# Kernel optimization log

Hardware: AMD Instinct MI355X
Metric: run time of the kernel (lower is better)

Reference implementation:

```python
import jax, jax.numpy as jnp
import numpy as np

N_NODES = 10000
N_EDGES = 160000
HIDDEN = 128
NGAUSS = 100
NF = 64
N_CONV = 2


def setup_inputs() -> dict:
    key = jax.random.key(0)
    ks = jax.random.split(key, 10)
    h = jax.random.normal(ks[0], (N_NODES, HIDDEN), dtype=jnp.float32)
    edge_index = jax.random.randint(ks[1], (2, N_EDGES), 0, N_NODES, dtype=jnp.int64)
    edge_weight = jax.random.uniform(ks[2], (N_EDGES,), dtype=jnp.float32)
    edge_attr = jax.random.normal(ks[3], (N_EDGES, NGAUSS), dtype=jnp.float32)
    data = jnp.zeros((1,), dtype=jnp.float32)
    s = 0.05
    lin0_w = jax.random.normal(ks[4], (HIDDEN, NF), dtype=jnp.float32) * s
    lin0_b = jnp.zeros((NF,), dtype=jnp.float32)
    nn_w1 = jax.random.normal(ks[5], (NGAUSS, HIDDEN), dtype=jnp.float32) * s
    nn_b1 = jnp.zeros((HIDDEN,), dtype=jnp.float32)
    nn_w2 = jax.random.normal(ks[6], (HIDDEN, NF * NF), dtype=jnp.float32) * s
    nn_b2 = jnp.zeros((NF * NF,), dtype=jnp.float32)
    root_w = jax.random.normal(ks[7], (NF, NF), dtype=jnp.float32) * s
    conv_b = jnp.zeros((NF,), dtype=jnp.float32)
    return {"h": h, "edge_index": edge_index, "edge_weight": edge_weight,
            "edge_attr": edge_attr, "data": data,
            "lin0_w": lin0_w, "lin0_b": lin0_b,
            "nn_w1": nn_w1, "nn_b1": nn_b1, "nn_w2": nn_w2, "nn_b2": nn_b2,
            "root_w": root_w, "conv_b": conv_b}


def reference(h, edge_index, edge_weight, edge_attr, data,
              lin0_w, lin0_b, nn_w1, nn_b1, nn_w2, nn_b2, root_w, conv_b):
    # lin0 + relu -> node features x: [N, nf]
    x = jax.nn.relu(h @ lin0_w + lin0_b)

    # edge network: per-edge weight matrix W_e: [E, nf, nf]
    hidden = jax.nn.relu(edge_attr @ nn_w1 + nn_b1)
    W_e = (hidden @ nn_w2 + nn_b2).reshape(N_EDGES, NF, NF)

    src = edge_index[0]  # message source (x_j)
    dst = edge_index[1]  # aggregation target (i)

    # in-degree for mean aggregation (0-degree nodes -> 0 output)
    deg = jax.ops.segment_sum(jnp.ones((N_EDGES,), x.dtype), dst, num_segments=N_NODES)
    inv_deg = (1.0 / jnp.maximum(deg, 1.0))[:, None]  # [N, 1]

    # n_conv applications of the SAME NNConv (shared weights)
    for _ in range(N_CONV):
        msg = jnp.einsum('ei,eio->eo', x[src], W_e)  # gather + per-edge matvec
        agg = jax.ops.segment_sum(msg, dst, num_segments=N_NODES) * inv_deg
        x = agg + x @ root_w + conv_b
    return x
```

## Files before the change

### kernel.cpp

```cpp
#include <hip/hip_runtime.h>

#define N_NODES 10000
#define N_EDGES 160000
#define HID 128
#define NG 100
#define NF 64
#define NIO 4096
#define NJ 8192
#define M_PAD 10240

#define PREP_EA 10000
#define PREP_LIN0 (PREP_EA + 2500)
#define PREP_WPT (PREP_LIN0 + 2112)

typedef short bf16x8 __attribute__((ext_vector_type(8)));
typedef float f32x4 __attribute__((ext_vector_type(4)));

__device__ __forceinline__ unsigned short f2b(float f) {
    unsigned int u = __float_as_uint(f);
    u += 0x7fffu + ((u >> 16) & 1u);
    return (unsigned short)(u >> 16);
}
__device__ __forceinline__ float b2f(unsigned short s) { return __uint_as_float((unsigned int)s << 16); }

__device__ __forceinline__ long fidx64(int row, int k) {
    return (long)(row >> 4) * 1024 + (k >> 5) * 512 + ((((k >> 3) & 3) * 16 + (row & 15))) * 8 + (k & 7);
}
__device__ __forceinline__ long fidx128(int row, int k) {
    return (long)(row >> 4) * 2048 + (k >> 5) * 512 + ((((k >> 3) & 3) * 16 + (row & 15))) * 8 + (k & 7);
}

__global__ void hist_kernel(const int* __restrict__ src, const int* __restrict__ dst,
                            float* __restrict__ deg, int* __restrict__ cnt) {
    int e = blockIdx.x * 256 + threadIdx.x;
    if (e < N_EDGES) {
        atomicAdd(&deg[dst[e]], 1.0f);
        atomicAdd(&cnt[src[e]], 1);
    }
}

#define SCAN_C 40
__global__ void scan_kernel(const int* __restrict__ cnt, const float* __restrict__ deg,
                            int* __restrict__ rowptr, float* __restrict__ invd) {
    __shared__ int wsum[4];
    int t = threadIdx.x, wv = t >> 6, l = t & 63;
    int base_i = t * SCAN_C;
    int loc[SCAN_C];
    int sum = 0;
#pragma unroll
    for (int j = 0; j < SCAN_C; ++j) {
        int g = base_i + j;
        int v = (g < N_NODES) ? cnt[g] : 0;
        loc[j] = sum;
        sum += v;
    }
    int incl = sum;
    for (int off = 1; off < 64; off <<= 1) {
        int v = __shfl_up(incl, off);
        if (l >= off) incl += v;
    }
    if (l == 63) wsum[wv] = incl;
    __syncthreads();
    int wbase = 0;
#pragma unroll
    for (int w = 0; w < 4; ++w) wbase += (w < wv) ? wsum[w] : 0;
    int tbase = wbase + incl - sum;
#pragma unroll
    for (int j = 0; j < SCAN_C; ++j) {
        int g = base_i + j;
        if (g <= N_NODES) rowptr[g] = tbase + loc[j];
        if (g < N_NODES) invd[g] = 1.0f / fmaxf(deg[g], 1.0f);
    }
}

__global__ void scatter_kernel(const int* __restrict__ src, const int* __restrict__ dst,
                               const int* __restrict__ rowptr, int* __restrict__ fill,
                               int* __restrict__ edgeOf, int* __restrict__ dstp) {
    int e = blockIdx.x * 256 + threadIdx.x;
    if (e < N_EDGES) {
        int s = src[e];
        int r = rowptr[s] + atomicAdd(&fill[s], 1);
        edgeOf[r] = e;
        dstp[r] = dst[e];
    }
}

__global__ void prep_kernel(const float* __restrict__ ea, const int* __restrict__ edgeOf,
                            unsigned short* __restrict__ eah,
                            const float* __restrict__ h, const float* __restrict__ lw,
                            const float* __restrict__ lb, const float* __restrict__ b2,
                            float* __restrict__ x, unsigned short* __restrict__ xh,
                            float* __restrict__ xb2,
                            const float* __restrict__ w1, const float* __restrict__ w2,
                            unsigned short* __restrict__ w1h, unsigned short* __restrict__ w2h) {
    int bid = blockIdx.x;
    if (bid < PREP_EA) {
        int t = threadIdx.x;
        int r15 = t & 15, ksl = t >> 4;
        int ks = ksl >> 2, lk = ksl & 3;
        long rank = (long)bid * 16 + r15;
        long e = edgeOf[rank];
        int c0 = ks * 32 + lk * 8;
        unsigned int uh[4];
#pragma unroll
        for (int p = 0; p < 4; ++p) {
            float v0 = (c0 + 2 * p < NG) ? ea[e * NG + c0 + 2 * p] : 0.0f;
            float v1 = (c0 + 2 * p + 1 < NG) ? ea[e * NG + c0 + 2 * p + 1] : 0.0f;
            uh[p] = ((unsigned int)f2b(v1) << 16) | f2b(v0);
        }
        long idx = (long)bid * 2048 + ks * 512 + (lk * 16 + r15) * 8;
        *(uint4*)(eah + idx) = make_uint4(uh[0], uh[1], uh[2], uh[3]);
    } else if (bid < PREP_LIN0) {
        int wv = threadIdx.x >> 6, l = threadIdx.x & 63;
        int n = (bid - PREP_EA) * 4 + wv;
        float h0 = h[n * HID + l];
        float h1 = h[n * HID + 64 + l];
        float acc = lb[l];
#pragma unroll
        for (int i = 0; i < 64; ++i) {
            acc += __shfl(h0, i) * lw[i * NF + l];
            acc += __shfl(h1, i) * lw[(64 + i) * NF + l];
        }
        float v = fmaxf(acc, 0.0f);
        x[n * NF + l] = v;
        xh[fidx64(n, l)] = f2b(v);
        float xb = 0.0f;
#pragma unroll
        for (int i = 0; i < 64; ++i) xb += __shfl(v, i) * b2[i * 64 + l];
        xb2[n * NF + l] = xb;
    } else {
        int id = (bid - PREP_LIN0) * 256 + threadIdx.x;
        if (id < HID * HID) {
            int k = id & 127, c = id >> 7;
            float v = (k < NG) ? w1[k * HID + c] : 0.0f;
            w1h[fidx128(c, k)] = f2b(v);
        } else {
            int id2 = id - HID * HID;
            int i = id2 & 63, j = id2 >> 6;
            int o = j >> 7, k = j & 127;
            w2h[fidx64(j, i)] = f2b(w2[k * NIO + i * 64 + o]);
        }
    }
}

__launch_bounds__(256)
__global__ void hgemm_kernel(const unsigned short* __restrict__ eah,
                             const unsigned short* __restrict__ w1h,
                             const float* __restrict__ b1, unsigned short* __restrict__ hidp) {
    __shared__ float stg[4][1056];
    const int tid = threadIdx.x, wv = tid >> 6, l = tid & 63;
    const long grow = (long)blockIdx.x * 128;
    const int wr = (wv >> 1) * 64, wc = (wv & 1) * 64;
    const long apan0 = (grow >> 4) + (wr >> 4);
    const long bpan0 = (wc >> 4);

    f32x4 acc[4][4] = {};
#pragma unroll
    for (int ks = 0; ks < 4; ++ks) {
        bf16x8 a[4], b[4];
#pragma unroll
        for (int m = 0; m < 4; ++m)
            a[m] = *(const bf16x8*)(eah + (apan0 + m) * 2048 + ks * 512 + (long)l * 8);
#pragma unroll
        for (int n = 0; n < 4; ++n)
            b[n] = *(const bf16x8*)(w1h + (bpan0 + n) * 2048 + ks * 512 + (long)l * 8);
#pragma unroll
        for (int m = 0; m < 4; ++m)
#pragma unroll
            for (int n = 0; n < 4; ++n)
                acc[m][n] = __builtin_amdgcn_mfma_f32_16x16x32_bf16(a[m], b[n], acc[m][n], 0, 0, 0);
    }

    float* s = stg[wv];
    int r8 = l >> 3, cg = l & 7;
#pragma unroll
    for (int m = 0; m < 4; ++m) {
#pragma unroll
        for (int n = 0; n < 4; ++n)
#pragma unroll
            for (int q = 0; q < 4; ++q)
                s[((l >> 4) * 4 + q) * 66 + n * 16 + (l & 15)] = acc[m][n][q];
#pragma unroll
        for (int it = 0; it < 2; ++it) {
            int row = it * 8 + r8;
            const float* sr = s + row * 66 + cg * 8;
            int colbase = wc + cg * 8;
            unsigned int u[4];
#pragma unroll
            for (int p = 0; p < 4; ++p) {
                float f0 = fmaxf(sr[2 * p] + b1[colbase + 2 * p], 0.0f);
                float f1 = fmaxf(sr[2 * p + 1] + b1[colbase + 2 * p + 1], 0.0f);
                u[p] = ((unsigned int)f2b(f1) << 16) | f2b(f0);
            }
            long R = grow + wr + m * 16 + row;
            *(uint4*)(hidp + R * HID + colbase) = make_uint4(u[0], u[1], u[2], u[3]);
        }
    }
}

__launch_bounds__(256)
__global__ void ygemm_kernel(const unsigned short* __restrict__ xh,
                             const unsigned short* __restrict__ wh,
                             unsigned short* __restrict__ y, int n0) {
    __shared__ float stg[4][1056];
    const int tid = threadIdx.x, wv = tid >> 6, l = tid & 63;
    const int grow = blockIdx.x * 128;
    const int col0base = blockIdx.y * 256;
    const int wr = (wv >> 1) * 64, wc = (wv & 1) * 64;
    const long apan0 = ((n0 + grow + wr) >> 4);
    const int r8 = l >> 3, cg = l & 7;

    bf16x8 a[2][4];
#pragma unroll
    for (int ks = 0; ks < 2; ++ks)
#pragma unroll
        for (int m = 0; m < 4; ++m)
            a[ks][m] = *(const bf16x8*)(xh + (apan0 + m) * 1024 + ks * 512 + (long)l * 8);

    for (int ct = 0; ct < 2; ++ct) {
        const int col0 = col0base + ct * 128;
        const long bpan0 = ((col0 + wc) >> 4);
        f32x4 acc[4][4] = {};
#pragma unroll
        for (int ks = 0; ks < 2; ++ks) {
            bf16x8 b[4];
#pragma unroll
            for (int n = 0; n < 4; ++n)
                b[n] = *(const bf16x8*)(wh + (bpan0 + n) * 1024 + ks * 512 + (long)l * 8);
#pragma unroll
            for (int m = 0; m < 4; ++m)
#pragma unroll
                for (int n = 0; n < 4; ++n)
                    acc[m][n] = __builtin_amdgcn_mfma_f32_16x16x32_bf16(a[ks][m], b[n], acc[m][n], 0, 0, 0);
        }

        float* s = stg[wv];
#pragma unroll
        for (int m = 0; m < 4; ++m) {
#pragma unroll
            for (int n = 0; n < 4; ++n)
#pragma unroll
                for (int q = 0; q < 4; ++q)
                    s[((l >> 4) * 4 + q) * 66 + n * 16 + (l & 15)] = acc[m][n][q];
#pragma unroll
            for (int it = 0; it < 2; ++it) {
                int row = it * 8 + r8;
                const float* sr = s + row * 66 + cg * 8;
                unsigned int u[4];
#pragma unroll
                for (int p = 0; p < 4; ++p)
                    u[p] = ((unsigned int)f2b(sr[2 * p + 1]) << 16) | f2b(sr[2 * p]);
                long R = grow + wr + m * 16 + row;
                *(uint4*)(y + R * NJ + col0 + wc + cg * 8) = make_uint4(u[0], u[1], u[2], u[3]);
            }
        }
    }
}

__global__ void matvec_mfma_kernel(const unsigned short* __restrict__ y,
                                   const unsigned short* __restrict__ hidp,
                                   const int* __restrict__ rowptr, const int* __restrict__ dstp,
                                   const float* __restrict__ xb2, float* __restrict__ agg,
                                   int n0, int n1) {
    int wv = threadIdx.x >> 6, l = threadIdx.x & 63;
    int s = n0 + blockIdx.x * 4 + wv;
    if (s >= n1) return;
    int r0 = rowptr[s], r1 = rowptr[s + 1];
    if (r0 == r1) return;
    int lc = l & 15, lk = l >> 4;

    const unsigned short* Ys = y + (long)(s - n0) * NJ;
    bf16x8 b[4][4];
    float xb2v[4];
#pragma unroll
    for (int og = 0; og < 4; ++og) {
        const unsigned short* Yo = Ys + (og * 16 + lc) * HID + lk * 8;
#pragma unroll
        for (int ks = 0; ks < 4; ++ks) b[og][ks] = *(const bf16x8*)(Yo + ks * 32);
        xb2v[og] = xb2[(long)s * NF + og * 16 + lc];
    }

    for (int mt = r0; mt < r1; mt += 16) {
        const unsigned short* Hs = hidp + (long)(mt + lc) * HID + lk * 8;
        bf16x8 a[4];
#pragma unroll
        for (int ks = 0; ks < 4; ++ks) a[ks] = *(const bf16x8*)(Hs + ks * 32);
        f32x4 acc[4] = {};
#pragma unroll
        for (int og = 0; og < 4; ++og)
#pragma unroll
            for (int ks = 0; ks < 4; ++ks)
                acc[og] = __builtin_amdgcn_mfma_f32_16x16x32_bf16(a[ks], b[og][ks], acc[og], 0, 0, 0);
#pragma unroll
        for (int q = 0; q < 4; ++q) {
            int rank = mt + lk * 4 + q;
            if (rank < r1) {
                long base = (long)dstp[rank] * NF;
#pragma unroll
                for (int og = 0; og < 4; ++og)
                    atomicAdd(&agg[base + og * 16 + lc], acc[og][q] + xb2v[og]);
            }
        }
    }
}

__global__ void combine_kernel(const float* __restrict__ x, float* __restrict__ agg,
                               const float* __restrict__ invd, const float* __restrict__ rw,
                               const float* __restrict__ cb, const float* __restrict__ b2,
                               float* __restrict__ xo, unsigned short* __restrict__ xh,
                               float* __restrict__ xb2) {
    int wv = threadIdx.x >> 6, l = threadIdx.x & 63;
    int n = blockIdx.x * 4 + wv;
    float xv = x[n * NF + l];
    float acc = cb[l];
#pragma unroll
    for (int i = 0; i < 64; ++i) acc += __shfl(xv, i) * rw[i * NF + l];
    float av = agg[n * NF + l];
    agg[n * NF + l] = 0.0f;
    float v = av * invd[n] + acc;
    xo[n * NF + l] = v;
    if (xh) {
        xh[fidx64(n, l)] = f2b(v);
        float xb = 0.0f;
#pragma unroll
        for (int i = 0; i < 64; ++i) xb += __shfl(v, i) * b2[i * 64 + l];
        xb2[n * NF + l] = xb;
    }
}

extern "C" void kernel_launch(void* const* d_in, const int* in_sizes, int n_in,
                              void* d_out, int out_size, void* d_ws, size_t ws_size,
                              hipStream_t stream) {
    const float* h = (const float*)d_in[0];
    const int* ei = (const int*)d_in[1];
    const float* ea = (const float*)d_in[3];
    const float* lin0_w = (const float*)d_in[5];
    const float* lin0_b = (const float*)d_in[6];
    const float* nn_w1 = (const float*)d_in[7];
    const float* nn_b1 = (const float*)d_in[8];
    const float* nn_w2 = (const float*)d_in[9];
    const float* nn_b2 = (const float*)d_in[10];
    const float* root_w = (const float*)d_in[11];
    const float* conv_b = (const float*)d_in[12];
    const int* srcIdx = ei;
    const int* dstIdx = ei + N_EDGES;

    const size_t eaBytes = (size_t)N_EDGES * HID * 2;
    const size_t fixed =
        (size_t)(N_EDGES + 16) * HID * 2 +
        (size_t)NJ * NF * 2 +
        (size_t)HID * HID * 2 +
        (size_t)M_PAD * NF * 2 +
        (size_t)N_NODES * NF * 4 * 4 +
        3 * 40192 +
        (size_t)N_NODES * 4 +
        (size_t)(N_NODES + 1) * 4 +
        (size_t)N_EDGES * 4 * 2 +
        32768;
    int nc = 0, CSn = 0;
    size_t region_bytes = 0;
    for (int c = 2; c <= 16; c *= 2) {
        int csn = (((N_NODES + c - 1) / c) + 127) & ~127;
        size_t rb = (size_t)csn * NJ * 2;
        if (rb < eaBytes) rb = eaBytes;
        if (fixed + rb <= ws_size) { nc = c; CSn = csn; region_bytes = rb; break; }
    }
    if (nc == 0) {
        hipMemsetAsync(d_out, 0, (size_t)out_size * 4, stream);
        return;
    }

    char* ws = (char*)d_ws;
    size_t off = 0;
    auto alloc = [&](size_t bytes) {
        char* p = ws + off;
        off += (bytes + 255) & ~(size_t)255;
        return p;
    };
    unsigned short* region = (unsigned short*)alloc(region_bytes);
    unsigned short* y = region;
    unsigned short* eah = region;
    unsigned short* hidp = (unsigned short*)alloc((size_t)(N_EDGES + 16) * HID * 2);
    unsigned short* w2h = (unsigned short*)alloc((size_t)NJ * NF * 2);
    unsigned short* w1h = (unsigned short*)alloc((size_t)HID * HID * 2);
    unsigned short* xh = (unsigned short*)alloc((size_t)M_PAD * NF * 2);
    float* xA = (float*)alloc((size_t)N_NODES * NF * 4);
    float* xB = (float*)alloc((size_t)N_NODES * NF * 4);
    float* agg = (float*)alloc((size_t)N_NODES * NF * 4);
    float* xb2 = (float*)alloc((size_t)N_NODES * NF * 4);
    char* degblk = alloc(3 * 40192);
    float* deg = (float*)degblk;
    int* cnt = (int*)(degblk + 40192);
    int* fill = (int*)(degblk + 2 * 40192);
    float* invd = (float*)alloc((size_t)N_NODES * 4);
    int* rowptr = (int*)alloc((size_t)(N_NODES + 1) * 4);
    int* edgeOf = (int*)alloc((size_t)N_EDGES * 4);
    int* dstp = (int*)alloc((size_t)N_EDGES * 4);

    hipMemsetAsync(degblk, 0, 3 * 40192, stream);
    hipMemsetAsync(agg, 0, (size_t)N_NODES * NF * 4, stream);
    hist_kernel<<<(N_EDGES + 255) / 256, 256, 0, stream>>>(srcIdx, dstIdx, deg, cnt);
    scan_kernel<<<1, 256, 0, stream>>>(cnt, deg, rowptr, invd);
    scatter_kernel<<<(N_EDGES + 255) / 256, 256, 0, stream>>>(srcIdx, dstIdx, rowptr, fill, edgeOf, dstp);
    prep_kernel<<<PREP_WPT, 256, 0, stream>>>(ea, edgeOf, eah,
                                              h, lin0_w, lin0_b, nn_b2, xA, xh, xb2,
                                              nn_w1, nn_w2, w1h, w2h);
    hgemm_kernel<<<N_EDGES / 128, 256, 0, stream>>>(eah, w1h, nn_b1, hidp);

    for (int conv = 0; conv < 2; ++conv) {
        const float* xin = conv ? xB : xA;
        float* xout = conv ? (float*)d_out : xB;
        unsigned short* mh = conv ? nullptr : xh;

        for (int c = 0; c < nc; ++c) {
            int n0 = c * CSn;
            int n1 = n0 + CSn; if (n1 > N_NODES) n1 = N_NODES;
            if (n0 >= N_NODES) break;
            int gx = (n1 - n0 + 127) / 128;
            ygemm_kernel<<<dim3(gx, NJ / 256), 256, 0, stream>>>(xh, w2h, y, n0);
            matvec_mfma_kernel<<<(n1 - n0 + 3) / 4, 256, 0, stream>>>(y, hidp, rowptr, dstp,
                                                                      xb2, agg, n0, n1);
        }
        combine_kernel<<<N_NODES / 4, 256, 0, stream>>>(xin, agg, invd, root_w, conv_b, nn_b2,
                                                        xout, mh, xb2);
    }
}
```

Measured before the change: 348.4 us.

## Fuse edge-attr bf16 conversion into hidden GEMM with scattered output rows

Removes the edge_attr permute-and-convert pass from the prep kernel. The hidden-layer GEMM now reads fp32 edge_attr directly in original edge order, converts it to bf16 in registers, and writes each output row to its source-sorted rank through a new rankOf array produced by the scatter kernel. This avoids writing and re-reading a 40MB bf16 intermediate and the gather by edgeOf. In exchange the GEMM does unaligned fp32 row loads, since rows are 100 floats, and its output stores become scattered.

```diff
diff --git a/kernel.cpp b/kernel.cpp
--- a/kernel.cpp
+++ b/kernel.cpp
@@ -9,8 +9,7 @@
 #define NJ 8192
 #define M_PAD 10240
 
-#define PREP_EA 10000
-#define PREP_LIN0 (PREP_EA + 2500)
+#define PREP_LIN0 2500
 #define PREP_WPT (PREP_LIN0 + 2112)
 
 typedef short bf16x8 __attribute__((ext_vector_type(8)));
@@ -75,44 +74,26 @@
 
 __global__ void scatter_kernel(const int* __restrict__ src, const int* __restrict__ dst,
                                const int* __restrict__ rowptr, int* __restrict__ fill,
-                               int* __restrict__ edgeOf, int* __restrict__ dstp) {
+                               int* __restrict__ rankOf, int* __restrict__ dstp) {
     int e = blockIdx.x * 256 + threadIdx.x;
     if (e < N_EDGES) {
         int s = src[e];
         int r = rowptr[s] + atomicAdd(&fill[s], 1);
-        edgeOf[r] = e;
+        rankOf[e] = r;
         dstp[r] = dst[e];
     }
 }
 
-__global__ void prep_kernel(const float* __restrict__ ea, const int* __restrict__ edgeOf,
-                            unsigned short* __restrict__ eah,
-                            const float* __restrict__ h, const float* __restrict__ lw,
+__global__ void prep_kernel(const float* __restrict__ h, const float* __restrict__ lw,
                             const float* __restrict__ lb, const float* __restrict__ b2,
                             float* __restrict__ x, unsigned short* __restrict__ xh,
                             float* __restrict__ xb2,
                             const float* __restrict__ w1, const float* __restrict__ w2,
                             unsigned short* __restrict__ w1h, unsigned short* __restrict__ w2h) {
     int bid = blockIdx.x;
-    if (bid < PREP_EA) {
-        int t = threadIdx.x;
-        int r15 = t & 15, ksl = t >> 4;
-        int ks = ksl >> 2, lk = ksl & 3;
-        long rank = (long)bid * 16 + r15;
-        long e = edgeOf[rank];
-        int c0 = ks * 32 + lk * 8;
-        unsigned int uh[4];
-#pragma unroll
-        for (int p = 0; p < 4; ++p) {
-            float v0 = (c0 + 2 * p < NG) ? ea[e * NG + c0 + 2 * p] : 0.0f;
-            float v1 = (c0 + 2 * p + 1 < NG) ? ea[e * NG + c0 + 2 * p + 1] : 0.0f;
-            uh[p] = ((unsigned int)f2b(v1) << 16) | f2b(v0);
-        }
-        long idx = (long)bid * 2048 + ks * 512 + (lk * 16 + r15) * 8;
-        *(uint4*)(eah + idx) = make_uint4(uh[0], uh[1], uh[2], uh[3]);
-    } else if (bid < PREP_LIN0) {
+    if (bid < PREP_LIN0) {
         int wv = threadIdx.x >> 6, l = threadIdx.x & 63;
-        int n = (bid - PREP_EA) * 4 + wv;
+        int n = bid * 4 + wv;
         float h0 = h[n * HID + l];
         float h1 = h[n * HID + 64 + l];
         float acc = lb[l];
@@ -144,23 +125,36 @@
 }
 
 __launch_bounds__(256)
-__global__ void hgemm_kernel(const unsigned short* __restrict__ eah,
+__global__ void hgemm_kernel(const float* __restrict__ ea, const int* __restrict__ rankOf,
                              const unsigned short* __restrict__ w1h,
                              const float* __restrict__ b1, unsigned short* __restrict__ hidp) {
     __shared__ float stg[4][1056];
     const int tid = threadIdx.x, wv = tid >> 6, l = tid & 63;
     const long grow = (long)blockIdx.x * 128;
     const int wr = (wv >> 1) * 64, wc = (wv & 1) * 64;
-    const long apan0 = (grow >> 4) + (wr >> 4);
     const long bpan0 = (wc >> 4);
+    const int lc = l & 15, lk = l >> 4;
 
     f32x4 acc[4][4] = {};
 #pragma unroll
     for (int ks = 0; ks < 4; ++ks) {
+        const int c0 = ks * 32 + lk * 8;
         bf16x8 a[4], b[4];
 #pragma unroll
-        for (int m = 0; m < 4; ++m)
-            a[m] = *(const bf16x8*)(eah + (apan0 + m) * 2048 + ks * 512 + (long)l * 8);
+        for (int m = 0; m < 4; ++m) {
+            const float* Ar = ea + (grow + wr + m * 16 + lc) * (long)NG;
+            f32x4 lo = {0.0f, 0.0f, 0.0f, 0.0f}, hi = {0.0f, 0.0f, 0.0f, 0.0f};
+            if (c0 <= 88) {
+                lo = *(const f32x4*)(Ar + c0);
+                hi = *(const f32x4*)(Ar + c0 + 4);
+            } else if (c0 == 96) {
+                lo = *(const f32x4*)(Ar + 96);
+            }
+            bf16x8 t;
+            t[0] = f2b(lo[0]); t[1] = f2b(lo[1]); t[2] = f2b(lo[2]); t[3] = f2b(lo[3]);
+            t[4] = f2b(hi[0]); t[5] = f2b(hi[1]); t[6] = f2b(hi[2]); t[7] = f2b(hi[3]);
+            a[m] = t;
+        }
 #pragma unroll
         for (int n = 0; n < 4; ++n)
             b[n] = *(const bf16x8*)(w1h + (bpan0 + n) * 2048 + ks * 512 + (long)l * 8);
@@ -192,8 +186,9 @@
                 float f1 = fmaxf(sr[2 * p + 1] + b1[colbase + 2 * p + 1], 0.0f);
                 u[p] = ((unsigned int)f2b(f1) << 16) | f2b(f0);
             }
-            long R = grow + wr + m * 16 + row;
-            *(uint4*)(hidp + R * HID + colbase) = make_uint4(u[0], u[1], u[2], u[3]);
+            long Redge = grow + wr + m * 16 + row;
+            long Ro = rankOf[Redge];
+            *(uint4*)(hidp + Ro * HID + colbase) = make_uint4(u[0], u[1], u[2], u[3]);
         }
     }
 }
@@ -345,7 +340,6 @@
     const int* srcIdx = ei;
     const int* dstIdx = ei + N_EDGES;
 
-    const size_t eaBytes = (size_t)N_EDGES * HID * 2;
     const size_t fixed =
         (size_t)(N_EDGES + 16) * HID * 2 +
         (size_t)NJ * NF * 2 +
@@ -362,7 +356,6 @@
     for (int c = 2; c <= 16; c *= 2) {
         int csn = (((N_NODES + c - 1) / c) + 127) & ~127;
         size_t rb = (size_t)csn * NJ * 2;
-        if (rb < eaBytes) rb = eaBytes;
         if (fixed + rb <= ws_size) { nc = c; CSn = csn; region_bytes = rb; break; }
     }
     if (nc == 0) {
@@ -377,9 +370,7 @@
         off += (bytes + 255) & ~(size_t)255;
         return p;
     };
-    unsigned short* region = (unsigned short*)alloc(region_bytes);
-    unsigned short* y = region;
-    unsigned short* eah = region;
+    unsigned short* y = (unsigned short*)alloc(region_bytes);
     unsigned short* hidp = (unsigned short*)alloc((size_t)(N_EDGES + 16) * HID * 2);
     unsigned short* w2h = (unsigned short*)alloc((size_t)NJ * NF * 2);
     unsigned short* w1h = (unsigned short*)alloc((size_t)HID * HID * 2);
@@ -394,18 +385,17 @@
     int* fill = (int*)(degblk + 2 * 40192);
     float* invd = (float*)alloc((size_t)N_NODES * 4);
     int* rowptr = (int*)alloc((size_t)(N_NODES + 1) * 4);
-    int* edgeOf = (int*)alloc((size_t)N_EDGES * 4);
+    int* rankOf = (int*)alloc((size_t)N_EDGES * 4);
     int* dstp = (int*)alloc((size_t)N_EDGES * 4);
 
     hipMemsetAsync(degblk, 0, 3 * 40192, stream);
     hipMemsetAsync(agg, 0, (size_t)N_NODES * NF * 4, stream);
     hist_kernel<<<(N_EDGES + 255) / 256, 256, 0, stream>>>(srcIdx, dstIdx, deg, cnt);
     scan_kernel<<<1, 256, 0, stream>>>(cnt, deg, rowptr, invd);
-    scatter_kernel<<<(N_EDGES + 255) / 256, 256, 0, stream>>>(srcIdx, dstIdx, rowptr, fill, edgeOf, dstp);
-    prep_kernel<<<PREP_WPT, 256, 0, stream>>>(ea, edgeOf, eah,
-                                              h, lin0_w, lin0_b, nn_b2, xA, xh, xb2,
+    scatter_kernel<<<(N_EDGES + 255) / 256, 256, 0, stream>>>(srcIdx, dstIdx, rowptr, fill, rankOf, dstp);
+    prep_kernel<<<PREP_WPT, 256, 0, stream>>>(h, lin0_w, lin0_b, nn_b2, xA, xh, xb2,
                                               nn_w1, nn_w2, w1h, w2h);
-    hgemm_kernel<<<N_EDGES / 128, 256, 0, stream>>>(eah, w1h, nn_b1, hidp);
+    hgemm_kernel<<<N_EDGES / 128, 256, 0, stream>>>(ea, rankOf, w1h, nn_b1, hidp);
 
     for (int conv = 0; conv < 2; ++conv) {
         const float* xin = conv ? xB : xA;
```

Measured after the change: 333.3 us, median of 2. -4.3%, faster.
